# Optimization experiments

Measured on AMD Instinct MI355X. Metric: run time of the kernel, lower is better.

## Reference

```python
import jax, jax.numpy as jnp
import numpy as np

B, C, H, W = 16, 384, 32, 32
K = 3  # depthwise kernel size


def setup_inputs() -> dict:
    key = jax.random.key(0)
    k1, k2, k3, k4, k5 = jax.random.split(key, 5)
    x = jax.random.normal(k1, (B, C, H, W), dtype=jnp.float32)
    # nn.Linear(C, 3C): weight [3C, C], bias [3C]
    lim = 1.0 / np.sqrt(C)
    w_qkv = jax.random.uniform(k2, (3 * C, C), minval=-lim, maxval=lim, dtype=jnp.float32)
    b_qkv = jax.random.uniform(k3, (3 * C,), minval=-lim, maxval=lim, dtype=jnp.float32)
    # depthwise Conv2d(C, C, K, padding=K//2, groups=C): weight [C, 1, K, K], bias [C]
    lim_c = 1.0 / np.sqrt(K * K)
    w_dw = jax.random.uniform(k4, (C, 1, K, K), minval=-lim_c, maxval=lim_c, dtype=jnp.float32)
    b_dw = jax.random.uniform(k5, (C,), minval=-lim_c, maxval=lim_c, dtype=jnp.float32)
    return {"x": x, "w_qkv": w_qkv, "b_qkv": b_qkv, "w_dw": w_dw, "b_dw": b_dw}


def _forward(x, w_qkv, b_qkv, w_dw, b_dw):
    Bx, Cx, Hx, Wx = x.shape
    N = Hx * Wx
    # x_flat: [B, N, C]
    x_flat = x.reshape(Bx, Cx, N).transpose(0, 2, 1)
    # qkv projection: [B, N, 3C] -> q, k, v each [B, N, C]
    qkv = jnp.einsum('bnc,oc->bno', x_flat, w_qkv) + b_qkv
    q, k, v = jnp.split(qkv, 3, axis=-1)
    # depthwise conv relative bias: [B, C, H, W] -> [B, N, C]
    rb = jax.lax.conv_general_dilated(
        x, w_dw, window_strides=(1, 1), padding='SAME',
        dimension_numbers=('NCHW', 'OIHW', 'NCHW'), feature_group_count=Cx)
    rb = rb + b_dw[None, :, None, None]
    rb = rb.reshape(Bx, Cx, N).transpose(0, 2, 1)
    # attention logits: q@k^T + q@rb^T == q @ (k + rb)^T  (no scaling in original)
    attn = jnp.einsum('bqc,bkc->bqk', q, k + rb)
    attn = jax.nn.softmax(attn, axis=-1)
    out_flat = jnp.einsum('bqk,bkc->bqc', attn, v)
    return out_flat.transpose(0, 2, 1).reshape(Bx, Cx, Hx, Wx)


def reference(x, w_qkv, b_qkv, w_dw, b_dw):
    return _forward(x, w_qkv, b_qkv, w_dw, b_dw)
```

## Files before the change

### kernel.cpp

```cpp
#include <hip/hip_runtime.h>

typedef _Float16 f16;
typedef _Float16 f16x8 __attribute__((ext_vector_type(8)));
typedef _Float16 f16x4 __attribute__((ext_vector_type(4)));
typedef _Float16 f16x2 __attribute__((ext_vector_type(2)));
typedef float f32x4 __attribute__((ext_vector_type(4)));

#define L2E 1.44269504088896f

typedef __attribute__((address_space(1))) void GV;
typedef __attribute__((address_space(3))) void LV;
__device__ __forceinline__ void gl2lds(const void* gp, void* lp) {
    __builtin_amdgcn_global_load_lds((GV*)gp, (LV*)lp, 16, 0, 0);
}

__global__ void k_wcvt(const float* __restrict__ w, f16* __restrict__ wh) {
    int i = (blockIdx.x * 256 + threadIdx.x) * 4;
    float4 v = *(const float4*)(w + i);
    f16x4 o = { (f16)v.x, (f16)v.y, (f16)v.z, (f16)v.w };
    *(f16x4*)(wh + i) = o;
}

__launch_bounds__(256)
__global__ void k_prep(const float* __restrict__ x, const float* __restrict__ wdw,
                       const float* __restrict__ bdw,
                       f16* __restrict__ xt, f16* __restrict__ rbt) {
    int ht = blockIdx.x, ct = blockIdx.y, b = blockIdx.z;
    __shared__ float xs[64 * 129];
    int t = threadIdx.x;
    int h0 = ht * 2;
#pragma unroll
    for (int i = 0; i < 8; ++i) {
        int idx = t + i * 256;
        int cl = idx >> 5, col4 = idx & 31;
        int hh = h0 - 1 + (col4 >> 3);
        int wq = (col4 & 7) * 4;
        float4 v = make_float4(0.f, 0.f, 0.f, 0.f);
        if (hh >= 0 && hh < 32)
            v = *(const float4*)(x + (size_t)(b * 384 + ct * 64 + cl) * 1024 + hh * 32 + wq);
        int base = cl * 129 + col4 * 4;
        xs[base] = v.x; xs[base + 1] = v.y; xs[base + 2] = v.z; xs[base + 3] = v.w;
    }
    __syncthreads();
    int cl = t & 63;
    int c = ct * 64 + cl;
    float wd[9];
#pragma unroll
    for (int k = 0; k < 9; ++k) wd[k] = wdw[c * 9 + k];
    float bd = bdw[c];
    const float* row = &xs[cl * 129];
    int nb = (t >> 6) * 16;
#pragma unroll
    for (int i = 0; i < 16; ++i) {
        int nl = nb + i;
        int hh = nl >> 5, ww = nl & 31;
        int lx = hh + 1;
        float acc = bd;
#pragma unroll
        for (int dh = -1; dh <= 1; ++dh) {
#pragma unroll
            for (int dw = -1; dw <= 1; ++dw) {
                int w2 = ww + dw;
                if (w2 >= 0 && w2 <= 31)
                    acc += wd[(dh + 1) * 3 + (dw + 1)] * row[(lx + dh) * 32 + w2];
            }
        }
        float xc = row[lx * 32 + ww];
        size_t at = ((size_t)(b * 1024) + h0 * 32 + nl) * 384 + c;
        rbt[at] = (f16)acc;
        xt[at] = (f16)xc;
    }
}

__launch_bounds__(256, 2)
__global__ void k_gemm1(const f16* __restrict__ xt, const f16* __restrict__ wh,
                        const float* __restrict__ bias, const f16* __restrict__ rbt,
                        f16* __restrict__ qo, f16* __restrict__ krb, f16* __restrict__ vt) {
    __shared__ f16 As[128 * 64];
    __shared__ f16 Bs[128 * 64];
    int bm = blockIdx.x, bn = blockIdx.y, b = blockIdx.z;
    int t = threadIdx.x, lane = t & 63, wv = t >> 6;
    int wm = wv >> 1, wn = wv & 1;
    f32x4 acc[4][4] = {};
    const char* xbase = (const char*)(xt + (size_t)(b * 1024 + bm * 128) * 384);
    const char* wbase = (const char*)(wh + (size_t)(bn * 128) * 384);
    const bool vmode = (bn >= 6);
    int soff[4];
#pragma unroll
    for (int i = 0; i < 4; ++i) {
        int idx = i * 256 + t;
        int r = idx >> 3, cg = idx & 7;
        soff[i] = r * 768 + ((cg ^ (r & 7)) << 4);
    }
    for (int kc = 0; kc < 6; ++kc) {
        __syncthreads();
#pragma unroll
        for (int i = 0; i < 4; ++i) {
            gl2lds(xbase + kc * 128 + soff[i], (char*)As + (i * 256 + wv * 64) * 16);
            gl2lds(wbase + kc * 128 + soff[i], (char*)Bs + (i * 256 + wv * 64) * 16);
        }
        __syncthreads();
#pragma unroll
        for (int j = 0; j < 2; ++j) {
            f16x8 af[4], bf[4];
#pragma unroll
            for (int mr = 0; mr < 4; ++mr) {
                int rowi = wm * 64 + mr * 16 + (lane & 15);
                af[mr] = *(const f16x8*)((const char*)As + rowi * 128 +
                         ((j * 64 + (lane >> 4) * 16) ^ ((rowi & 7) << 4)));
            }
#pragma unroll
            for (int nr = 0; nr < 4; ++nr) {
                int rowi = wn * 64 + nr * 16 + (lane & 15);
                bf[nr] = *(const f16x8*)((const char*)Bs + rowi * 128 +
                         ((j * 64 + (lane >> 4) * 16) ^ ((rowi & 7) << 4)));
            }
            __builtin_amdgcn_s_setprio(1);
            if (!vmode) {
#pragma unroll
                for (int mr = 0; mr < 4; ++mr)
#pragma unroll
                    for (int nr = 0; nr < 4; ++nr)
                        acc[mr][nr] = __builtin_amdgcn_mfma_f32_16x16x32_f16(af[mr], bf[nr], acc[mr][nr], 0, 0, 0);
            } else {
#pragma unroll
                for (int mr = 0; mr < 4; ++mr)
#pragma unroll
                    for (int nr = 0; nr < 4; ++nr)
                        acc[mr][nr] = __builtin_amdgcn_mfma_f32_16x16x32_f16(bf[nr], af[mr], acc[mr][nr], 0, 0, 0);
            }
            __builtin_amdgcn_s_setprio(0);
        }
    }
    int o0 = bn * 128;
    if (!vmode) {
#pragma unroll
        for (int nr = 0; nr < 4; ++nr) {
            int o = o0 + wn * 64 + nr * 16 + (lane & 15);
            float bs = bias[o];
#pragma unroll
            for (int mr = 0; mr < 4; ++mr) {
                int n_l = wm * 64 + mr * 16 + ((lane >> 4) << 2);
#pragma unroll
                for (int r = 0; r < 4; ++r) {
                    int n_sp = bm * 128 + n_l + r;
                    size_t at = (size_t)(b * 1024 + n_sp) * 384;
                    float vv = acc[mr][nr][r] + bs;
                    if (o < 384) qo[at + o] = (f16)vv;
                    else krb[at + (o - 384)] = (f16)(vv + (float)rbt[at + (o - 384)]);
                }
            }
        }
    } else {
#pragma unroll
        for (int nr = 0; nr < 4; ++nr) {
#pragma unroll
            for (int mr = 0; mr < 4; ++mr) {
                int n_sp = bm * 128 + wm * 64 + mr * 16 + (lane & 15);
                int o_l = wn * 64 + nr * 16 + ((lane >> 4) << 2);
#pragma unroll
                for (int r = 0; r < 4; ++r) {
                    float vv = acc[mr][nr][r] + bias[o0 + o_l + r];
                    vt[(size_t)(b * 384 + (o0 - 768) + o_l + r) * 1024 + n_sp] = (f16)vv;
                }
            }
        }
    }
}

__launch_bounds__(256, 1)
__global__ void k_flash3(const f16* __restrict__ q, const f16* __restrict__ krb,
                         const f16* __restrict__ vt, float* __restrict__ out) {
    __shared__ char smem[49152];
    char* Ks = smem;
    char* Vs = smem + 24576;
    int qt = blockIdx.x, b = blockIdx.y;
    int t = threadIdx.x, lane = t & 63, wv = t >> 6;
    int g = lane >> 4, ln = lane & 15;
    int n0 = qt * 64;

    f16x8 qf[12];
    {
        const f16* qb = q + (size_t)(b * 1024 + n0 + wv * 16 + ln) * 384 + g * 8;
#pragma unroll
        for (int kc = 0; kc < 12; ++kc) qf[kc] = *(const f16x8*)(qb + kc * 32);
    }

    int koff[6], voff[6];
#pragma unroll
    for (int i = 0; i < 6; ++i) {
        int idx = i * 256 + t;
        int r = idx / 48, c = idx - r * 48;
        koff[i] = r * 768 + ((c ^ (r & 7)) << 4);
        int vr = idx >> 2, vc = idx & 3;
        voff[i] = vr * 2048 + ((vc ^ (vr & 3)) << 4);
    }
    const char* kbase = (const char*)(krb + (size_t)b * 1024 * 384);
    const char* vbase = (const char*)(vt + (size_t)b * 384 * 1024);

#pragma unroll
    for (int i = 0; i < 6; ++i)
        gl2lds(kbase + koff[i], Ks + (i * 256 + wv * 64) * 16);

    f32x4 oa[24];
#pragma unroll
    for (int i = 0; i < 24; ++i) oa[i] = (f32x4){0.f, 0.f, 0.f, 0.f};
    float m_run = -1e30f, l_run = 0.f;
    int src0 = 2 * (g & 1) * 16 + ln, src1 = src0 + 16;
    bool gh = (g >= 2);

    for (int kt = 0; kt < 32; ++kt) {
        __syncthreads();
#pragma unroll
        for (int i = 0; i < 6; ++i)
            gl2lds(vbase + kt * 64 + voff[i], Vs + (i * 256 + wv * 64) * 16);

        f32x4 st[2] = {};
        __builtin_amdgcn_s_setprio(1);
#pragma unroll
        for (int kc = 0; kc < 12; ++kc) {
#pragma unroll
            for (int nr = 0; nr < 2; ++nr) {
                int kvr = nr * 16 + ln;
                f16x8 kf = *(const f16x8*)(Ks + kvr * 768 +
                            ((kc * 64 + g * 16) ^ ((kvr & 7) << 4)));
                st[nr] = __builtin_amdgcn_mfma_f32_16x16x32_f16(kf, qf[kc], st[nr], 0, 0, 0);
            }
        }
        __builtin_amdgcn_s_setprio(0);

        float mx = st[0][0];
#pragma unroll
        for (int nr = 0; nr < 2; ++nr)
#pragma unroll
            for (int r = 0; r < 4; ++r) mx = fmaxf(mx, st[nr][r]);
        mx = fmaxf(mx, __shfl_xor(mx, 16));
        mx = fmaxf(mx, __shfl_xor(mx, 32));
        float mn = fmaxf(m_run, mx);
        float sc = exp2f((m_run - mn) * L2E);
        m_run = mn;
        float ls = 0.f;
        float pv[2][4];
#pragma unroll
        for (int nr = 0; nr < 2; ++nr)
#pragma unroll
            for (int r = 0; r < 4; ++r) {
                float p = exp2f((st[nr][r] - mn) * L2E);
                pv[nr][r] = p;
                ls += p;
            }
        ls += __shfl_xor(ls, 16);
        ls += __shfl_xor(ls, 32);
        l_run = l_run * sc + ls;
#pragma unroll
        for (int i = 0; i < 24; ++i) oa[i] *= sc;

        int pk[4];
#pragma unroll
        for (int nr = 0; nr < 2; ++nr)
#pragma unroll
            for (int h = 0; h < 2; ++h) {
                f16x2 w2 = { (f16)pv[nr][2 * h], (f16)pv[nr][2 * h + 1] };
                pk[nr * 2 + h] = __builtin_bit_cast(int, w2);
            }
        f16x8 pb;
        {
            int a0 = __shfl(pk[0], src0);
            int a1 = __shfl(pk[1], src0);
            int a2 = __shfl(pk[2], src0);
            int a3 = __shfl(pk[3], src0);
            int b0 = __shfl(pk[0], src1);
            int b1 = __shfl(pk[1], src1);
            int b2 = __shfl(pk[2], src1);
            int b3 = __shfl(pk[3], src1);
            union { int w[4]; f16x8 v; } u;
            u.w[0] = gh ? a2 : a0;
            u.w[1] = gh ? a3 : a1;
            u.w[2] = gh ? b2 : b0;
            u.w[3] = gh ? b3 : b1;
            pb = u.v;
        }

        __syncthreads();
        if (kt < 31) {
#pragma unroll
            for (int i = 0; i < 6; ++i)
                gl2lds(kbase + (kt + 1) * 24576 + koff[i], Ks + (i * 256 + wv * 64) * 16);
        }

        __builtin_amdgcn_s_setprio(1);
#pragma unroll
        for (int nr2 = 0; nr2 < 24; ++nr2) {
            int cr = nr2 * 16 + ln;
            f16x8 vf = *(const f16x8*)(Vs + cr * 64 +
                        ((g * 16) ^ ((cr & 3) << 4)));
            oa[nr2] = __builtin_amdgcn_mfma_f32_16x16x32_f16(vf, pb, oa[nr2], 0, 0, 0);
        }
        __builtin_amdgcn_s_setprio(0);
    }

    float inv = 1.0f / l_run;
#pragma unroll
    for (int nr2 = 0; nr2 < 24; ++nr2) {
#pragma unroll
        for (int r = 0; r < 4; ++r) {
            int c = nr2 * 16 + g * 4 + r;
            out[(size_t)(b * 384 + c) * 1024 + n0 + wv * 16 + ln] = oa[nr2][r] * inv;
        }
    }
}

extern "C" void kernel_launch(void* const* d_in, const int* in_sizes, int n_in,
                              void* d_out, int out_size, void* d_ws, size_t ws_size,
                              hipStream_t stream) {
    const float* x     = (const float*)d_in[0];
    const float* w_qkv = (const float*)d_in[1];
    const float* b_qkv = (const float*)d_in[2];
    const float* w_dw  = (const float*)d_in[3];
    const float* b_dw  = (const float*)d_in[4];
    float* out = (float*)d_out;
    char* ws = (char*)d_ws;
    const size_t SZ = (size_t)16 * 1024 * 384 * 2;
    f16* xt  = (f16*)(ws);
    f16* rbt = (f16*)(ws + SZ);
    f16* qo  = (f16*)(ws + 2 * SZ);
    f16* krb = (f16*)(ws + 3 * SZ);
    f16* vt  = (f16*)(ws + 4 * SZ);
    f16* wh  = (f16*)(ws + 5 * SZ);

    k_wcvt<<<432, 256, 0, stream>>>(w_qkv, wh);
    k_prep<<<dim3(16, 6, 16), 256, 0, stream>>>(x, w_dw, b_dw, xt, rbt);
    k_gemm1<<<dim3(8, 9, 16), 256, 0, stream>>>(xt, wh, b_qkv, rbt, qo, krb, vt);
    k_flash3<<<dim3(16, 16), 256, 0, stream>>>(qo, krb, vt, out);
}
```

Measured before the change: 207.1 us.

## Split KV range across warp halves in flash kernel and merge partial softmax states

The flash attention kernel now processes 32 queries per block instead of 64, and splits the 1024 keys into two halves handled by separate warp pairs with their own LDS buffers. The partial (max, sum, accumulator) states are combined through shared memory at the end. This doubles the grid to 512 blocks and allows two blocks per CU, which should improve occupancy and latency hiding. It also adds a lazy rescale that skips the accumulator rescale when the new max stays within a threshold of the running max, and uses a 16x16x16 MFMA for PV to avoid the P shuffle. The cost is an extra LDS merge step and the narrower 16x16x16 MFMA.

```diff
diff --git a/kernel.cpp b/kernel.cpp
--- a/kernel.cpp
+++ b/kernel.cpp
@@ -168,144 +168,135 @@
     }
 }
 
-__launch_bounds__(256, 1)
-__global__ void k_flash3(const f16* __restrict__ q, const f16* __restrict__ krb,
+__launch_bounds__(256, 2)
+__global__ void k_flash4(const f16* __restrict__ q, const f16* __restrict__ krb,
                          const f16* __restrict__ vt, float* __restrict__ out) {
     __shared__ char smem[49152];
-    char* Ks = smem;
-    char* Vs = smem + 24576;
+    __shared__ float mlb[32][2];
     int qt = blockIdx.x, b = blockIdx.y;
     int t = threadIdx.x, lane = t & 63, wv = t >> 6;
     int g = lane >> 4, ln = lane & 15;
-    int n0 = qt * 64;
+    int h = wv >> 1, qw = wv & 1;
+    char* Ks = smem + h * 12288;
+    char* Vs = smem + 24576 + h * 12288;
 
     f16x8 qf[12];
     {
-        const f16* qb = q + (size_t)(b * 1024 + n0 + wv * 16 + ln) * 384 + g * 8;
+        const f16* qb = q + (size_t)(b * 1024 + qt * 32 + qw * 16 + ln) * 384 + g * 8;
 #pragma unroll
         for (int kc = 0; kc < 12; ++kc) qf[kc] = *(const f16x8*)(qb + kc * 32);
     }
 
+    int tp = t & 127;
     int koff[6], voff[6];
 #pragma unroll
     for (int i = 0; i < 6; ++i) {
-        int idx = i * 256 + t;
+        int idx = i * 128 + tp;
         int r = idx / 48, c = idx - r * 48;
         koff[i] = r * 768 + ((c ^ (r & 7)) << 4);
-        int vr = idx >> 2, vc = idx & 3;
-        voff[i] = vr * 2048 + ((vc ^ (vr & 3)) << 4);
-    }
-    const char* kbase = (const char*)(krb + (size_t)b * 1024 * 384);
-    const char* vbase = (const char*)(vt + (size_t)b * 384 * 1024);
+        int vr = idx >> 1, vc = idx & 1;
+        voff[i] = vr * 2048 + ((vc ^ ((vr >> 2) & 1)) << 4);
+    }
+    const char* kbase = (const char*)krb + (size_t)b * 786432 + (size_t)(h * 512) * 768;
+    const char* vbase = (const char*)vt + (size_t)b * 786432 + (size_t)(h * 512) * 2;
 
 #pragma unroll
     for (int i = 0; i < 6; ++i)
-        gl2lds(kbase + koff[i], Ks + (i * 256 + wv * 64) * 16);
+        gl2lds(kbase + koff[i], Ks + (i * 128 + qw * 64) * 16);
 
     f32x4 oa[24];
 #pragma unroll
     for (int i = 0; i < 24; ++i) oa[i] = (f32x4){0.f, 0.f, 0.f, 0.f};
     float m_run = -1e30f, l_run = 0.f;
-    int src0 = 2 * (g & 1) * 16 + ln, src1 = src0 + 16;
-    bool gh = (g >= 2);
 
     for (int kt = 0; kt < 32; ++kt) {
         __syncthreads();
 #pragma unroll
         for (int i = 0; i < 6; ++i)
-            gl2lds(vbase + kt * 64 + voff[i], Vs + (i * 256 + wv * 64) * 16);
-
-        f32x4 st[2] = {};
+            gl2lds(vbase + kt * 32 + voff[i], Vs + (i * 128 + qw * 64) * 16);
+
+        f32x4 st = {};
         __builtin_amdgcn_s_setprio(1);
 #pragma unroll
         for (int kc = 0; kc < 12; ++kc) {
-#pragma unroll
-            for (int nr = 0; nr < 2; ++nr) {
-                int kvr = nr * 16 + ln;
-                f16x8 kf = *(const f16x8*)(Ks + kvr * 768 +
-                            ((kc * 64 + g * 16) ^ ((kvr & 7) << 4)));
-                st[nr] = __builtin_amdgcn_mfma_f32_16x16x32_f16(kf, qf[kc], st[nr], 0, 0, 0);
-            }
+            f16x8 kf = *(const f16x8*)(Ks + ln * 768 +
+                        ((kc * 64 + g * 16) ^ ((ln & 7) << 4)));
+            st = __builtin_amdgcn_mfma_f32_16x16x32_f16(kf, qf[kc], st, 0, 0, 0);
         }
         __builtin_amdgcn_s_setprio(0);
 
-        float mx = st[0][0];
-#pragma unroll
-        for (int nr = 0; nr < 2; ++nr)
-#pragma unroll
-            for (int r = 0; r < 4; ++r) mx = fmaxf(mx, st[nr][r]);
+        float mx = fmaxf(fmaxf(st[0], st[1]), fmaxf(st[2], st[3]));
         mx = fmaxf(mx, __shfl_xor(mx, 16));
         mx = fmaxf(mx, __shfl_xor(mx, 32));
-        float mn = fmaxf(m_run, mx);
-        float sc = exp2f((m_run - mn) * L2E);
-        m_run = mn;
-        float ls = 0.f;
-        float pv[2][4];
-#pragma unroll
-        for (int nr = 0; nr < 2; ++nr)
-#pragma unroll
-            for (int r = 0; r < 4; ++r) {
-                float p = exp2f((st[nr][r] - mn) * L2E);
-                pv[nr][r] = p;
-                ls += p;
-            }
+        float mn;
+        if (__all(mx <= m_run + 8.0f)) {
+            mn = m_run;
+        } else {
+            mn = fmaxf(m_run, mx);
+            float sc = exp2f((m_run - mn) * L2E);
+            m_run = mn;
+            l_run *= sc;
+#pragma unroll
+            for (int i = 0; i < 24; ++i) oa[i] *= sc;
+        }
+        float p[4], ls = 0.f;
+#pragma unroll
+        for (int r = 0; r < 4; ++r) {
+            p[r] = exp2f((st[r] - mn) * L2E);
+            ls += p[r];
+        }
         ls += __shfl_xor(ls, 16);
         ls += __shfl_xor(ls, 32);
-        l_run = l_run * sc + ls;
-#pragma unroll
-        for (int i = 0; i < 24; ++i) oa[i] *= sc;
-
-        int pk[4];
-#pragma unroll
-        for (int nr = 0; nr < 2; ++nr)
-#pragma unroll
-            for (int h = 0; h < 2; ++h) {
-                f16x2 w2 = { (f16)pv[nr][2 * h], (f16)pv[nr][2 * h + 1] };
-                pk[nr * 2 + h] = __builtin_bit_cast(int, w2);
-            }
-        f16x8 pb;
-        {
-            int a0 = __shfl(pk[0], src0);
-            int a1 = __shfl(pk[1], src0);
-            int a2 = __shfl(pk[2], src0);
-            int a3 = __shfl(pk[3], src0);
-            int b0 = __shfl(pk[0], src1);
-            int b1 = __shfl(pk[1], src1);
-            int b2 = __shfl(pk[2], src1);
-            int b3 = __shfl(pk[3], src1);
-            union { int w[4]; f16x8 v; } u;
-            u.w[0] = gh ? a2 : a0;
-            u.w[1] = gh ? a3 : a1;
-            u.w[2] = gh ? b2 : b0;
-            u.w[3] = gh ? b3 : b1;
-            pb = u.v;
-        }
+        l_run += ls;
+        f16x4 pb = { (f16)p[0], (f16)p[1], (f16)p[2], (f16)p[3] };
 
         __syncthreads();
         if (kt < 31) {
 #pragma unroll
             for (int i = 0; i < 6; ++i)
-                gl2lds(kbase + (kt + 1) * 24576 + koff[i], Ks + (i * 256 + wv * 64) * 16);
+                gl2lds(kbase + (kt + 1) * 12288 + koff[i], Ks + (i * 128 + qw * 64) * 16);
         }
 
         __builtin_amdgcn_s_setprio(1);
 #pragma unroll
         for (int nr2 = 0; nr2 < 24; ++nr2) {
-            int cr = nr2 * 16 + ln;
-            f16x8 vf = *(const f16x8*)(Vs + cr * 64 +
-                        ((g * 16) ^ ((cr & 3) << 4)));
-            oa[nr2] = __builtin_amdgcn_mfma_f32_16x16x32_f16(vf, pb, oa[nr2], 0, 0, 0);
+            int c = nr2 * 16 + ln;
+            f16x4 vf = *(const f16x4*)(Vs + c * 32 +
+                        ((g ^ (((c >> 2) & 1) << 1)) << 3));
+            oa[nr2] = __builtin_amdgcn_mfma_f32_16x16x16f16(vf, pb, oa[nr2], 0, 0, 0);
         }
         __builtin_amdgcn_s_setprio(0);
     }
 
-    float inv = 1.0f / l_run;
-#pragma unroll
-    for (int nr2 = 0; nr2 < 24; ++nr2) {
-#pragma unroll
-        for (int r = 0; r < 4; ++r) {
-            int c = nr2 * 16 + g * 4 + r;
-            out[(size_t)(b * 384 + c) * 1024 + n0 + wv * 16 + ln] = oa[nr2][r] * inv;
+    __syncthreads();
+    float* ob = (float*)smem;
+    if (h == 1) {
+        if (g == 0) {
+            mlb[qw * 16 + ln][0] = m_run;
+            mlb[qw * 16 + ln][1] = l_run;
+        }
+#pragma unroll
+        for (int nr2 = 0; nr2 < 24; ++nr2)
+#pragma unroll
+            for (int r = 0; r < 4; ++r)
+                ob[(nr2 * 16 + g * 4 + r) * 32 + qw * 16 + ln] = oa[nr2][r];
+    }
+    __syncthreads();
+    if (h == 0) {
+        int qq = qw * 16 + ln;
+        float mB = mlb[qq][0], lB = mlb[qq][1];
+        float M = fmaxf(m_run, mB);
+        float eA = exp2f((m_run - M) * L2E);
+        float eB = exp2f((mB - M) * L2E);
+        float linv = 1.0f / (l_run * eA + lB * eB);
+#pragma unroll
+        for (int nr2 = 0; nr2 < 24; ++nr2) {
+#pragma unroll
+            for (int r = 0; r < 4; ++r) {
+                int c = nr2 * 16 + g * 4 + r;
+                out[(size_t)(b * 384 + c) * 1024 + qt * 32 + qq] =
+                    (oa[nr2][r] * eA + ob[c * 32 + qq] * eB) * linv;
+            }
         }
     }
 }
@@ -331,5 +322,5 @@
     k_wcvt<<<432, 256, 0, stream>>>(w_qkv, wh);
     k_prep<<<dim3(16, 6, 16), 256, 0, stream>>>(x, w_dw, b_dw, xt, rbt);
     k_gemm1<<<dim3(8, 9, 16), 256, 0, stream>>>(xt, wh, b_qkv, rbt, qo, krb, vt);
-    k_flash3<<<dim3(16, 16), 256, 0, stream>>>(qo, krb, vt, out);
-}
+    k_flash4<<<dim3(32, 16), 256, 0, stream>>>(qo, krb, vt, out);
+}
```

New measurement: 224.5 us. +8.4%, slower.

## Split KV range across wave pairs with LDS merge, stream V from global

Applied to the files above, without the earlier changes.

The flash attention kernel now uses 32-query tiles, which doubles the grid to 512 blocks. Two wave pairs each process half of the key sequence, and their partial softmax states are merged through LDS at the end. V is read straight from global memory instead of being staged in LDS. Online-softmax rescaling is skipped when the new max exceeds the running max by no more than 8. The goal is more parallelism and occupancy on 256 CUs, at the cost of uncoalesced V loads, extra merge work, and some risk to fp16 range from the lazy rescale.

```diff
diff --git a/kernel.cpp b/kernel.cpp
--- a/kernel.cpp
+++ b/kernel.cpp
@@ -168,39 +168,38 @@
     }
 }
 
-__launch_bounds__(256, 1)
-__global__ void k_flash3(const f16* __restrict__ q, const f16* __restrict__ krb,
+__launch_bounds__(256, 2)
+__global__ void k_flash5(const f16* __restrict__ q, const f16* __restrict__ krb,
                          const f16* __restrict__ vt, float* __restrict__ out) {
     __shared__ char smem[49152];
-    char* Ks = smem;
-    char* Vs = smem + 24576;
+    __shared__ float mlb[32][2];
     int qt = blockIdx.x, b = blockIdx.y;
     int t = threadIdx.x, lane = t & 63, wv = t >> 6;
     int g = lane >> 4, ln = lane & 15;
-    int n0 = qt * 64;
+    int h = wv >> 1, qw = wv & 1;
+    char* Ks = smem + h * 24576;
 
     f16x8 qf[12];
     {
-        const f16* qb = q + (size_t)(b * 1024 + n0 + wv * 16 + ln) * 384 + g * 8;
+        const f16* qb = q + (size_t)(b * 1024 + qt * 32 + qw * 16 + ln) * 384 + g * 8;
 #pragma unroll
         for (int kc = 0; kc < 12; ++kc) qf[kc] = *(const f16x8*)(qb + kc * 32);
     }
 
-    int koff[6], voff[6];
-#pragma unroll
-    for (int i = 0; i < 6; ++i) {
-        int idx = i * 256 + t;
+    int tp = t & 127;
+    int koff[12];
+#pragma unroll
+    for (int i = 0; i < 12; ++i) {
+        int idx = i * 128 + tp;
         int r = idx / 48, c = idx - r * 48;
         koff[i] = r * 768 + ((c ^ (r & 7)) << 4);
-        int vr = idx >> 2, vc = idx & 3;
-        voff[i] = vr * 2048 + ((vc ^ (vr & 3)) << 4);
-    }
-    const char* kbase = (const char*)(krb + (size_t)b * 1024 * 384);
-    const char* vbase = (const char*)(vt + (size_t)b * 384 * 1024);
-
-#pragma unroll
-    for (int i = 0; i < 6; ++i)
-        gl2lds(kbase + koff[i], Ks + (i * 256 + wv * 64) * 16);
+    }
+    const char* kbase = (const char*)krb + (size_t)b * 786432 + (size_t)h * 393216;
+    const f16* vbase = vt + (size_t)b * 384 * 1024 + h * 512;
+
+#pragma unroll
+    for (int i = 0; i < 12; ++i)
+        gl2lds(kbase + koff[i], Ks + (i * 128 + qw * 64) * 16);
 
     f32x4 oa[24];
 #pragma unroll
@@ -209,12 +208,8 @@
     int src0 = 2 * (g & 1) * 16 + ln, src1 = src0 + 16;
     bool gh = (g >= 2);
 
-    for (int kt = 0; kt < 32; ++kt) {
+    for (int kt = 0; kt < 16; ++kt) {
         __syncthreads();
-#pragma unroll
-        for (int i = 0; i < 6; ++i)
-            gl2lds(vbase + kt * 64 + voff[i], Vs + (i * 256 + wv * 64) * 16);
-
         f32x4 st[2] = {};
         __builtin_amdgcn_s_setprio(1);
 #pragma unroll
@@ -228,6 +223,12 @@
             }
         }
         __builtin_amdgcn_s_setprio(0);
+        __syncthreads();
+        if (kt < 15) {
+#pragma unroll
+            for (int i = 0; i < 12; ++i)
+                gl2lds(kbase + (kt + 1) * 24576 + koff[i], Ks + (i * 128 + qw * 64) * 16);
+        }
 
         float mx = st[0][0];
 #pragma unroll
@@ -236,11 +237,18 @@
             for (int r = 0; r < 4; ++r) mx = fmaxf(mx, st[nr][r]);
         mx = fmaxf(mx, __shfl_xor(mx, 16));
         mx = fmaxf(mx, __shfl_xor(mx, 32));
-        float mn = fmaxf(m_run, mx);
-        float sc = exp2f((m_run - mn) * L2E);
-        m_run = mn;
-        float ls = 0.f;
-        float pv[2][4];
+        float mn;
+        if (__all(mx <= m_run + 8.0f)) {
+            mn = m_run;
+        } else {
+            mn = fmaxf(m_run, mx);
+            float sc = exp2f((m_run - mn) * L2E);
+            m_run = mn;
+            l_run *= sc;
+#pragma unroll
+            for (int i = 0; i < 24; ++i) oa[i] *= sc;
+        }
+        float pv[2][4], ls = 0.f;
 #pragma unroll
         for (int nr = 0; nr < 2; ++nr)
 #pragma unroll
@@ -251,17 +259,15 @@
             }
         ls += __shfl_xor(ls, 16);
         ls += __shfl_xor(ls, 32);
-        l_run = l_run * sc + ls;
-#pragma unroll
-        for (int i = 0; i < 24; ++i) oa[i] *= sc;
+        l_run += ls;
 
         int pk[4];
 #pragma unroll
         for (int nr = 0; nr < 2; ++nr)
 #pragma unroll
-            for (int h = 0; h < 2; ++h) {
-                f16x2 w2 = { (f16)pv[nr][2 * h], (f16)pv[nr][2 * h + 1] };
-                pk[nr * 2 + h] = __builtin_bit_cast(int, w2);
+            for (int hh = 0; hh < 2; ++hh) {
+                f16x2 w2 = { (f16)pv[nr][2 * hh], (f16)pv[nr][2 * hh + 1] };
+                pk[nr * 2 + hh] = __builtin_bit_cast(int, w2);
             }
         f16x8 pb;
         {
@@ -281,31 +287,46 @@
             pb = u.v;
         }
 
-        __syncthreads();
-        if (kt < 31) {
-#pragma unroll
-            for (int i = 0; i < 6; ++i)
-                gl2lds(kbase + (kt + 1) * 24576 + koff[i], Ks + (i * 256 + wv * 64) * 16);
-        }
-
+        const f16* vrow = vbase + kt * 32 + g * 8;
         __builtin_amdgcn_s_setprio(1);
 #pragma unroll
         for (int nr2 = 0; nr2 < 24; ++nr2) {
             int cr = nr2 * 16 + ln;
-            f16x8 vf = *(const f16x8*)(Vs + cr * 64 +
-                        ((g * 16) ^ ((cr & 3) << 4)));
+            f16x8 vf = *(const f16x8*)(vrow + (size_t)cr * 1024);
             oa[nr2] = __builtin_amdgcn_mfma_f32_16x16x32_f16(vf, pb, oa[nr2], 0, 0, 0);
         }
         __builtin_amdgcn_s_setprio(0);
     }
 
-    float inv = 1.0f / l_run;
-#pragma unroll
-    for (int nr2 = 0; nr2 < 24; ++nr2) {
-#pragma unroll
-        for (int r = 0; r < 4; ++r) {
-            int c = nr2 * 16 + g * 4 + r;
-            out[(size_t)(b * 384 + c) * 1024 + n0 + wv * 16 + ln] = oa[nr2][r] * inv;
+    __syncthreads();
+    float* ob = (float*)smem;
+    if (h == 1) {
+        if (g == 0) {
+            mlb[qw * 16 + ln][0] = m_run;
+            mlb[qw * 16 + ln][1] = l_run;
+        }
+#pragma unroll
+        for (int nr2 = 0; nr2 < 24; ++nr2)
+#pragma unroll
+            for (int r = 0; r < 4; ++r)
+                ob[(nr2 * 16 + g * 4 + r) * 32 + qw * 16 + ln] = oa[nr2][r];
+    }
+    __syncthreads();
+    if (h == 0) {
+        int qq = qw * 16 + ln;
+        float mB = mlb[qq][0], lB = mlb[qq][1];
+        float M = fmaxf(m_run, mB);
+        float eA = exp2f((m_run - M) * L2E);
+        float eB = exp2f((mB - M) * L2E);
+        float linv = 1.0f / (l_run * eA + lB * eB);
+#pragma unroll
+        for (int nr2 = 0; nr2 < 24; ++nr2) {
+#pragma unroll
+            for (int r = 0; r < 4; ++r) {
+                int c = nr2 * 16 + g * 4 + r;
+                out[(size_t)(b * 384 + c) * 1024 + qt * 32 + qq] =
+                    (oa[nr2][r] * eA + ob[c * 32 + qq] * eB) * linv;
+            }
         }
     }
 }
@@ -331,5 +352,5 @@
     k_wcvt<<<432, 256, 0, stream>>>(w_qkv, wh);
     k_prep<<<dim3(16, 6, 16), 256, 0, stream>>>(x, w_dw, b_dw, xt, rbt);
     k_gemm1<<<dim3(8, 9, 16), 256, 0, stream>>>(xt, wh, b_qkv, rbt, qo, krb, vt);
-    k_flash3<<<dim3(16, 16), 256, 0, stream>>>(qo, krb, vt, out);
-}
+    k_flash5<<<dim3(32, 16), 256, 0, stream>>>(qo, krb, vt, out);
+}
```

After: 253.6 us. 22.4% more time.

## Enlarge GEMM tile to 256 rows with 512 threads and reswizzle V shared memory

Applied to the files above, without the earlier changes.

The QKV projection kernel now uses 512-thread blocks covering 256 spatial rows per block, so each weight tile loaded into shared memory is reused by eight waves instead of four and the grid halves. Separately, the flash kernel's V tile swizzle is changed to an XOR pattern mixing row bits (r + r>>2), intended to reduce LDS bank conflicts on the V fragment reads. The larger GEMM block raises shared memory and register pressure per block and may lower occupancy.

```diff
diff --git a/kernel.cpp b/kernel.cpp
--- a/kernel.cpp
+++ b/kernel.cpp
@@ -72,33 +72,40 @@
     }
 }
 
-__launch_bounds__(256, 2)
-__global__ void k_gemm1(const f16* __restrict__ xt, const f16* __restrict__ wh,
+__launch_bounds__(512, 2)
+__global__ void k_gemm2(const f16* __restrict__ xt, const f16* __restrict__ wh,
                         const float* __restrict__ bias, const f16* __restrict__ rbt,
                         f16* __restrict__ qo, f16* __restrict__ krb, f16* __restrict__ vt) {
-    __shared__ f16 As[128 * 64];
+    __shared__ f16 As[256 * 64];
     __shared__ f16 Bs[128 * 64];
     int bm = blockIdx.x, bn = blockIdx.y, b = blockIdx.z;
     int t = threadIdx.x, lane = t & 63, wv = t >> 6;
     int wm = wv >> 1, wn = wv & 1;
     f32x4 acc[4][4] = {};
-    const char* xbase = (const char*)(xt + (size_t)(b * 1024 + bm * 128) * 384);
+    const char* xbase = (const char*)(xt + (size_t)(b * 1024 + bm * 256) * 384);
     const char* wbase = (const char*)(wh + (size_t)(bn * 128) * 384);
     const bool vmode = (bn >= 6);
-    int soff[4];
+    int soffA[4], soffB[2];
 #pragma unroll
     for (int i = 0; i < 4; ++i) {
-        int idx = i * 256 + t;
+        int idx = i * 512 + t;
         int r = idx >> 3, cg = idx & 7;
-        soff[i] = r * 768 + ((cg ^ (r & 7)) << 4);
+        soffA[i] = r * 768 + ((cg ^ (r & 7)) << 4);
+    }
+#pragma unroll
+    for (int i = 0; i < 2; ++i) {
+        int idx = i * 512 + t;
+        int r = idx >> 3, cg = idx & 7;
+        soffB[i] = r * 768 + ((cg ^ (r & 7)) << 4);
     }
     for (int kc = 0; kc < 6; ++kc) {
         __syncthreads();
 #pragma unroll
-        for (int i = 0; i < 4; ++i) {
-            gl2lds(xbase + kc * 128 + soff[i], (char*)As + (i * 256 + wv * 64) * 16);
-            gl2lds(wbase + kc * 128 + soff[i], (char*)Bs + (i * 256 + wv * 64) * 16);
-        }
+        for (int i = 0; i < 4; ++i)
+            gl2lds(xbase + kc * 128 + soffA[i], (char*)As + (i * 512 + wv * 64) * 16);
+#pragma unroll
+        for (int i = 0; i < 2; ++i)
+            gl2lds(wbase + kc * 128 + soffB[i], (char*)Bs + (i * 512 + wv * 64) * 16);
         __syncthreads();
 #pragma unroll
         for (int j = 0; j < 2; ++j) {
@@ -143,7 +150,7 @@
                 int n_l = wm * 64 + mr * 16 + ((lane >> 4) << 2);
 #pragma unroll
                 for (int r = 0; r < 4; ++r) {
-                    int n_sp = bm * 128 + n_l + r;
+                    int n_sp = bm * 256 + n_l + r;
                     size_t at = (size_t)(b * 1024 + n_sp) * 384;
                     float vv = acc[mr][nr][r] + bs;
                     if (o < 384) qo[at + o] = (f16)vv;
@@ -156,7 +163,7 @@
         for (int nr = 0; nr < 4; ++nr) {
 #pragma unroll
             for (int mr = 0; mr < 4; ++mr) {
-                int n_sp = bm * 128 + wm * 64 + mr * 16 + (lane & 15);
+                int n_sp = bm * 256 + wm * 64 + mr * 16 + (lane & 15);
                 int o_l = wn * 64 + nr * 16 + ((lane >> 4) << 2);
 #pragma unroll
                 for (int r = 0; r < 4; ++r) {
@@ -169,7 +176,7 @@
 }
 
 __launch_bounds__(256, 1)
-__global__ void k_flash3(const f16* __restrict__ q, const f16* __restrict__ krb,
+__global__ void k_flash6(const f16* __restrict__ q, const f16* __restrict__ krb,
                          const f16* __restrict__ vt, float* __restrict__ out) {
     __shared__ char smem[49152];
     char* Ks = smem;
@@ -193,7 +200,8 @@
         int r = idx / 48, c = idx - r * 48;
         koff[i] = r * 768 + ((c ^ (r & 7)) << 4);
         int vr = idx >> 2, vc = idx & 3;
-        voff[i] = vr * 2048 + ((vc ^ (vr & 3)) << 4);
+        int sv = (vr + (vr >> 2)) & 3;
+        voff[i] = vr * 2048 + ((vc ^ sv) << 4);
     }
     const char* kbase = (const char*)(krb + (size_t)b * 1024 * 384);
     const char* vbase = (const char*)(vt + (size_t)b * 384 * 1024);
@@ -259,9 +267,9 @@
 #pragma unroll
         for (int nr = 0; nr < 2; ++nr)
 #pragma unroll
-            for (int h = 0; h < 2; ++h) {
-                f16x2 w2 = { (f16)pv[nr][2 * h], (f16)pv[nr][2 * h + 1] };
-                pk[nr * 2 + h] = __builtin_bit_cast(int, w2);
+            for (int hh = 0; hh < 2; ++hh) {
+                f16x2 w2 = { (f16)pv[nr][2 * hh], (f16)pv[nr][2 * hh + 1] };
+                pk[nr * 2 + hh] = __builtin_bit_cast(int, w2);
             }
         f16x8 pb;
         {
@@ -292,8 +300,8 @@
 #pragma unroll
         for (int nr2 = 0; nr2 < 24; ++nr2) {
             int cr = nr2 * 16 + ln;
-            f16x8 vf = *(const f16x8*)(Vs + cr * 64 +
-                        ((g * 16) ^ ((cr & 3) << 4)));
+            int sv = (cr + (cr >> 2)) & 3;
+            f16x8 vf = *(const f16x8*)(Vs + cr * 64 + ((g ^ sv) << 4));
             oa[nr2] = __builtin_amdgcn_mfma_f32_16x16x32_f16(vf, pb, oa[nr2], 0, 0, 0);
         }
         __builtin_amdgcn_s_setprio(0);
@@ -330,6 +338,6 @@
 
     k_wcvt<<<432, 256, 0, stream>>>(w_qkv, wh);
     k_prep<<<dim3(16, 6, 16), 256, 0, stream>>>(x, w_dw, b_dw, xt, rbt);
-    k_gemm1<<<dim3(8, 9, 16), 256, 0, stream>>>(xt, wh, b_qkv, rbt, qo, krb, vt);
-    k_flash3<<<dim3(16, 16), 256, 0, stream>>>(qo, krb, vt, out);
-}
+    k_gemm2<<<dim3(4, 9, 16), 512, 0, stream>>>(xt, wh, b_qkv, rbt, qo, krb, vt);
+    k_flash6<<<dim3(16, 16), 256, 0, stream>>>(qo, krb, vt, out);
+}
```

Result: no change. 210.4 us (+1.6%).
